# Kernel tuning notes

Measured on AMD Instinct MI355X. Metric: run time of the kernel, lower is better.

The kernel has to match this reference:

```python
import jax, jax.numpy as jnp
import numpy as np

D_I = 1024
D_O = 1024
B = 4
S = 4096

def setup_inputs() -> dict:
    key = jax.random.key(0)
    kx, kq, kk, kv = jax.random.split(key, 4)
    x = jax.random.normal(kx, (B, S, D_I), dtype=jnp.float32)
    # torch Linear(d_i, d_o) weight is [d_o, d_i]; we store transposed [d_i, d_o]
    sc = 1.0 / np.sqrt(D_I)
    Wq = jax.random.uniform(kq, (D_I, D_O), jnp.float32, -sc, sc)
    Wk = jax.random.uniform(kk, (D_I, D_O), jnp.float32, -sc, sc)
    Wv = jax.random.uniform(kv, (D_I, D_O), jnp.float32, -sc, sc)
    return {"x": x, "Wq": Wq, "Wk": Wk, "Wv": Wv}

def reference(x, Wq, Wk, Wv):
    # x: [B, S, d_i]
    q = jnp.einsum('bsd,de->bse', x, Wq)  # [B,S,d_o]
    k = jnp.einsum('bsd,de->bse', x, Wk)
    v = jnp.einsum('bsd,de->bse', x, Wv)
    scores = jnp.einsum('bqe,bke->bqk', q, k)  # [B,S,S]
    S_len = x.shape[1]
    causal = jnp.tril(jnp.ones((S_len, S_len), dtype=bool))  # keep lower tri
    scores = jnp.where(causal[None], scores, -jnp.inf)
    attn = jax.nn.softmax(scores / jnp.sqrt(jnp.float32(v.shape[-1])), axis=-1)
    # dropout p=0.0 -> identity
    return jnp.einsum('bqk,bke->bqe', attn, v)  # [B,S,d_o]
```

## Files before the change

### kernel.cpp

```cpp
#include <hip/hip_runtime.h>

typedef __bf16 bf16x8 __attribute__((ext_vector_type(8)));
typedef float f32x4 __attribute__((ext_vector_type(4)));

#define B_SZ 4
#define S_SZ 4096
#define D_SZ 1024
#define ELEMS_MAT ((size_t)B_SZ * S_SZ * D_SZ)

#define OFF_Q  ((size_t)0)
#define OFF_K  (ELEMS_MAT)
#define OFF_VT (2 * ELEMS_MAT)
#define ZONE   (3 * ELEMS_MAT)
#define OFF_XB (ZONE)
#define OFF_V  (ZONE + ELEMS_MAT)
#define OFF_WT (ZONE + 2 * ELEMS_MAT)
#define OFF_S  (ZONE)
#define S_BATCH ((size_t)8912896)

#define MFMA16(a, b, c) __builtin_amdgcn_mfma_f32_16x16x32_bf16((a), (b), (c), 0, 0, 0)

static __device__ __forceinline__ unsigned short f2bf(float f) {
  __bf16 h = (__bf16)f;
  return __builtin_bit_cast(unsigned short, h);
}

static __device__ __forceinline__ void async_lds16(const void* g, void* l) {
  __builtin_amdgcn_global_load_lds((__attribute__((address_space(1))) void*)g,
                                   (__attribute__((address_space(3))) void*)l, 16, 0, 0);
}

__global__ void cast_x_kernel(const float* __restrict__ x, unsigned short* __restrict__ xb) {
  size_t i = ((size_t)blockIdx.x * 256 + threadIdx.x) * 8;
  f32x4 a = *(const f32x4*)(x + i);
  f32x4 b = *(const f32x4*)(x + i + 4);
  bf16x8 o;
  o[0] = (__bf16)a[0]; o[1] = (__bf16)a[1]; o[2] = (__bf16)a[2]; o[3] = (__bf16)a[3];
  o[4] = (__bf16)b[0]; o[5] = (__bf16)b[1]; o[6] = (__bf16)b[2]; o[7] = (__bf16)b[3];
  *(bf16x8*)(xb + i) = o;
}

__global__ void cast_wt_kernel(const float* __restrict__ Wq, const float* __restrict__ Wk,
                               const float* __restrict__ Wv, unsigned short* __restrict__ Wt) {
  __shared__ float tl[64][65];
  const float* W = blockIdx.z == 0 ? Wq : (blockIdx.z == 1 ? Wk : Wv);
  unsigned short* out = Wt + (size_t)blockIdx.z * (size_t)D_SZ * (size_t)D_SZ;
  const int k0 = blockIdx.x * 64, n0 = blockIdx.y * 64;
  const int t = threadIdx.x;
  for (int i = t; i < 4096; i += 256) {
    int r = i >> 6, c = i & 63;
    tl[r][c] = W[(size_t)(k0 + r) * D_SZ + n0 + c];
  }
  __syncthreads();
  for (int i = t; i < 4096; i += 256) {
    int r = i >> 6, c = i & 63;
    out[(size_t)(n0 + r) * D_SZ + k0 + c] = f2bf(tl[c][r]);
  }
}

static __device__ __forceinline__ void stage_tile(const char* Asrc, size_t lda,
                                                  const char* Bsrc, size_t ldb,
                                                  unsigned short* ldsA, unsigned short* ldsB,
                                                  int tid) {
#pragma unroll
  for (int it = 0; it < 4; ++it) {
    int i = it * 512 + tid;
    int row = i >> 3;
    int scol = ((i & 7) ^ (row & 7)) << 4;
    async_lds16(Asrc + (size_t)row * lda + scol, (char*)ldsA + i * 16);
  }
#pragma unroll
  for (int it = 0; it < 4; ++it) {
    int i = it * 512 + tid;
    int row = i >> 3;
    int scol = ((i & 7) ^ (row & 7)) << 4;
    async_lds16(Bsrc + (size_t)row * ldb + scol, (char*)ldsB + i * 16);
  }
}

static __device__ __forceinline__ void compute_tile(const unsigned short* As,
                                                    const unsigned short* Bs,
                                                    int wm, int wn, int lr, int hi,
                                                    f32x4 acc[8][4]) {
  const char* Ab = (const char*)As;
  const char* Bb = (const char*)Bs;
#pragma unroll
  for (int q = 0; q < 4; ++q) {
    const int qm = q >> 1, qn = q & 1;
    bf16x8 af[4][2], bfr[2][2];
#pragma unroll
    for (int f = 0; f < 4; ++f) {
      const int r = wm * 128 + (qm * 4 + f) * 16 + lr;
#pragma unroll
      for (int kk = 0; kk < 2; ++kk)
        af[f][kk] = *(const bf16x8*)(Ab + r * 128 + ((kk * 64 + hi * 16) ^ ((r & 7) << 4)));
    }
#pragma unroll
    for (int f = 0; f < 2; ++f) {
      const int r = wn * 64 + (qn * 2 + f) * 16 + lr;
#pragma unroll
      for (int kk = 0; kk < 2; ++kk)
        bfr[f][kk] = *(const bf16x8*)(Bb + r * 128 + ((kk * 64 + hi * 16) ^ ((r & 7) << 4)));
    }
    __builtin_amdgcn_s_setprio(1);
#pragma unroll
    for (int kk = 0; kk < 2; ++kk)
#pragma unroll
      for (int f = 0; f < 4; ++f)
#pragma unroll
        for (int g = 0; g < 2; ++g)
          acc[qm * 4 + f][qn * 2 + g] = MFMA16(af[f][kk], bfr[g][kk], acc[qm * 4 + f][qn * 2 + g]);
    __builtin_amdgcn_s_setprio(0);
  }
}

static __device__ __forceinline__ void gemm_mainloop(const char* A, size_t lda,
                                                     const char* B, size_t ldb, int NT,
                                                     unsigned short sm[2][2][16384],
                                                     int tid, f32x4 acc[8][4]) {
  const int lane = tid & 63, w = tid >> 6;
  const int wm = w >> 2, wn = w & 3, lr = lane & 15, hi = lane >> 4;
  stage_tile(A, lda, B, ldb, sm[0][0], sm[0][1], tid);
  for (int t = 0; t < NT - 1; ++t) {
    const int cur = t & 1;
    stage_tile(A + (size_t)(t + 1) * 128, lda, B + (size_t)(t + 1) * 128, ldb,
               sm[cur ^ 1][0], sm[cur ^ 1][1], tid);
    asm volatile("s_waitcnt vmcnt(8)" ::: "memory");
    __builtin_amdgcn_s_barrier();
    compute_tile(sm[cur][0], sm[cur][1], wm, wn, lr, hi, acc);
    __builtin_amdgcn_s_barrier();
  }
  asm volatile("s_waitcnt vmcnt(0)" ::: "memory");
  __builtin_amdgcn_s_barrier();
  compute_tile(sm[(NT - 1) & 1][0], sm[(NT - 1) & 1][1], wm, wn, lr, hi, acc);
}

#define GEMM_PRE()                                    \
  __shared__ unsigned short sm[2][2][16384];          \
  const int tid = threadIdx.x;                        \
  f32x4 acc[8][4];                                    \
  {                                                   \
    const f32x4 z4 = {0.f, 0.f, 0.f, 0.f};            \
    _Pragma("unroll") for (int f = 0; f < 8; ++f)     \
      _Pragma("unroll") for (int g = 0; g < 4; ++g)   \
        acc[f][g] = z4;                               \
  }

#define EPI_IDX()                                     \
  const int lane = tid & 63, w = tid >> 6;            \
  const int wm = w >> 2, wn = w & 3;                  \
  const int lr = lane & 15, hi = lane >> 4;

__global__ __launch_bounds__(512, 2) void gemm_qkv256(const unsigned short* __restrict__ xb,
                                                      const unsigned short* __restrict__ Wt,
                                                      unsigned short* __restrict__ Q,
                                                      unsigned short* __restrict__ K,
                                                      unsigned short* __restrict__ V) {
  GEMM_PRE();
  const int bid = blockIdx.x;
  const int sw = (bid & 7) * 96 + (bid >> 3);
  const int mt = sw % 64, nt = sw / 64;
  const char* A = (const char*)xb + (size_t)mt * 256 * 2048;
  const char* Bp = (const char*)Wt + (size_t)nt * 256 * 2048;
  gemm_mainloop(A, 2048, Bp, 2048, 16, sm, tid, acc);
  EPI_IDX();
  unsigned short* Out = (nt >> 2) == 0 ? Q : ((nt >> 2) == 1 ? K : V);
  const int nb = (nt & 3) * 256;
#pragma unroll
  for (int f = 0; f < 8; ++f)
#pragma unroll
    for (int g = 0; g < 4; ++g)
#pragma unroll
      for (int j = 0; j < 4; ++j) {
        const int m = mt * 256 + wm * 128 + f * 16 + hi * 4 + j;
        const int n = nb + wn * 64 + g * 16 + lr;
        Out[(size_t)m * D_SZ + n] = f2bf(acc[f][g][j]);
      }
}

static __device__ __forceinline__ void stage_a256(const char* src, size_t ld, char* lds, int tid) {
#pragma unroll
  for (int it = 0; it < 4; ++it) {
    int i = it * 512 + tid;
    int row = i >> 3;
    int scol = ((i & 7) ^ (row & 7)) << 4;
    async_lds16(src + (size_t)row * ld + scol, lds + i * 16);
  }
}
static __device__ __forceinline__ void stage_b128(const char* src, size_t ld, char* lds, int tid) {
#pragma unroll
  for (int it = 0; it < 2; ++it) {
    int i = it * 512 + tid;
    int row = i >> 3;
    int scol = ((i & 7) ^ (row & 7)) << 4;
    async_lds16(src + (size_t)row * ld + scol, lds + i * 16);
  }
}

static __device__ __forceinline__ void compute_tile128(const unsigned short* As,
                                                       const unsigned short* Bs,
                                                       int wm, int wn, int lr, int hi,
                                                       f32x4 acc[8][2]) {
  const char* Ab = (const char*)As;
  const char* Bb = (const char*)Bs;
  bf16x8 bfr[2][2];
#pragma unroll
  for (int g = 0; g < 2; ++g) {
    const int r = wn * 32 + g * 16 + lr;
#pragma unroll
    for (int kk = 0; kk < 2; ++kk)
      bfr[g][kk] = *(const bf16x8*)(Bb + r * 128 + ((kk * 64 + hi * 16) ^ ((r & 7) << 4)));
  }
#pragma unroll
  for (int p = 0; p < 4; ++p) {
    bf16x8 af[2][2];
#pragma unroll
    for (int f = 0; f < 2; ++f) {
      const int r = wm * 128 + (p * 2 + f) * 16 + lr;
#pragma unroll
      for (int kk = 0; kk < 2; ++kk)
        af[f][kk] = *(const bf16x8*)(Ab + r * 128 + ((kk * 64 + hi * 16) ^ ((r & 7) << 4)));
    }
    __builtin_amdgcn_s_setprio(1);
#pragma unroll
    for (int kk = 0; kk < 2; ++kk)
#pragma unroll
      for (int f = 0; f < 2; ++f)
#pragma unroll
        for (int g = 0; g < 2; ++g)
          acc[p * 2 + f][g] = MFMA16(af[f][kk], bfr[g][kk], acc[p * 2 + f][g]);
    __builtin_amdgcn_s_setprio(0);
  }
}

static __device__ __forceinline__ void mainloop128(const char* A, size_t lda,
                                                   const char* B, size_t ldb, int NT,
                                                   unsigned short (*smA)[16384],
                                                   unsigned short (*smB)[8192],
                                                   int tid, f32x4 acc[8][2]) {
  const int lane = tid & 63, w = tid >> 6;
  const int wm = w >> 2, wn = w & 3, lr = lane & 15, hi = lane >> 4;
  stage_a256(A, lda, (char*)smA[0], tid);
  stage_b128(B, ldb, (char*)smB[0], tid);
  for (int t = 0; t < NT - 1; ++t) {
    const int cur = t & 1;
    stage_a256(A + (size_t)(t + 1) * 128, lda, (char*)smA[cur ^ 1], tid);
    stage_b128(B + (size_t)(t + 1) * 128, ldb, (char*)smB[cur ^ 1], tid);
    asm volatile("s_waitcnt vmcnt(6)" ::: "memory");
    __builtin_amdgcn_s_barrier();
    compute_tile128(smA[cur], smB[cur], wm, wn, lr, hi, acc);
    __builtin_amdgcn_s_barrier();
  }
  asm volatile("s_waitcnt vmcnt(0)" ::: "memory");
  __builtin_amdgcn_s_barrier();
  compute_tile128(smA[(NT - 1) & 1], smB[(NT - 1) & 1], wm, wn, lr, hi, acc);
}

__global__ void transpose_v_kernel(const unsigned short* __restrict__ V,
                                   unsigned short* __restrict__ Vt) {
  __shared__ unsigned short tl[64][65];
  const int s0 = blockIdx.x * 64, d0 = blockIdx.y * 64, b = blockIdx.z;
  const int t = threadIdx.x;
  const unsigned short* Vb = V + (size_t)b * S_SZ * D_SZ;
  unsigned short* Vo = Vt + (size_t)b * D_SZ * S_SZ;
  for (int i = t; i < 4096; i += 256) {
    int r = i >> 6, c = i & 63;
    tl[r][c] = Vb[(size_t)(s0 + r) * D_SZ + d0 + c];
  }
  __syncthreads();
  for (int i = t; i < 4096; i += 256) {
    int r = i >> 6, c = i & 63;
    Vo[(size_t)(d0 + r) * S_SZ + s0 + c] = tl[c][r];
  }
}

__global__ __launch_bounds__(512, 2) void s_gemm_bn128(const unsigned short* __restrict__ Q,
                                                       const unsigned short* __restrict__ K,
                                                       unsigned short* __restrict__ Sp) {
  __shared__ unsigned short smA[2][16384];
  __shared__ unsigned short smB[2][8192];
  const int tid = threadIdx.x;
  f32x4 acc[8][2];
  {
    const f32x4 z4 = {0.f, 0.f, 0.f, 0.f};
#pragma unroll
    for (int f = 0; f < 8; ++f)
#pragma unroll
      for (int g = 0; g < 2; ++g) acc[f][g] = z4;
  }
  const int bid = blockIdx.x;
  const int sw = (bid & 7) * 136 + (bid >> 3);
  const int b = sw / 272;
  const int r = sw % 272;
  int I = (int)((sqrtf(4.0f * r + 1.0f) - 1.0f) * 0.5f);
  while ((I + 1) * (I + 2) <= r) ++I;
  while (I * (I + 1) > r) --I;
  const int Jh = r - I * (I + 1);

  const char* A = (const char*)Q + ((size_t)b * S_SZ + (size_t)I * 256) * 2048;
  const char* Bp = (const char*)K + ((size_t)b * S_SZ + (size_t)Jh * 128) * 2048;
  mainloop128(A, 2048, Bp, 2048, 16, smA, smB, tid, acc);
  EPI_IDX();
  const int L = (I + 1) * 256;
  unsigned short* So = Sp + (size_t)b * S_BATCH + (size_t)(I * (I + 1) / 2) * 65536;
#pragma unroll
  for (int f = 0; f < 8; ++f)
#pragma unroll
    for (int g = 0; g < 2; ++g)
#pragma unroll
      for (int j = 0; j < 4; ++j) {
        const int m = wm * 128 + f * 16 + hi * 4 + j;
        const int n = Jh * 128 + wn * 32 + g * 16 + lr;
        float val = acc[f][g][j] * 0.03125f;
        if (n > I * 256 + m) val = -1e30f;
        So[(size_t)m * L + n] = f2bf(val);
      }
}

__global__ __launch_bounds__(256) void softmax_kernel(unsigned short* __restrict__ Sp) {
  const int w = threadIdx.x >> 6, lane = threadIdx.x & 63;
  const int rowflat = blockIdx.x * 4 + w;
  const int rr = 16383 - rowflat;
  const int b = rr >> 12, q = rr & 4095;
  const int I = q >> 8;
  const int L = (I + 1) << 8;
  unsigned short* base = Sp + (size_t)b * S_BATCH + (size_t)(I * (I + 1) / 2) * 65536 +
                         (size_t)(q & 255) * L;
  const int niter = (L + 511) >> 9;
  const __bf16 NEG = (__bf16)(-1e30f);
  bf16x8 v[8];
#pragma unroll
  for (int jt = 0; jt < 8; ++jt) {
    if (jt < niter) {
      const int off = jt * 512 + lane * 8;
      if (off < L) v[jt] = *(const bf16x8*)(base + off);
      else { bf16x8 fz; fz[0]=NEG;fz[1]=NEG;fz[2]=NEG;fz[3]=NEG;fz[4]=NEG;fz[5]=NEG;fz[6]=NEG;fz[7]=NEG; v[jt] = fz; }
    }
  }
  float m = -1e30f;
#pragma unroll
  for (int jt = 0; jt < 8; ++jt)
    if (jt < niter)
#pragma unroll
      for (int e = 0; e < 8; ++e) m = fmaxf(m, (float)v[jt][e]);
  m = fmaxf(m, __shfl_xor(m, 1));  m = fmaxf(m, __shfl_xor(m, 2));
  m = fmaxf(m, __shfl_xor(m, 4));  m = fmaxf(m, __shfl_xor(m, 8));
  m = fmaxf(m, __shfl_xor(m, 16)); m = fmaxf(m, __shfl_xor(m, 32));
  float l = 0.f;
#pragma unroll
  for (int jt = 0; jt < 8; ++jt)
    if (jt < niter)
#pragma unroll
      for (int e = 0; e < 8; ++e) l += __expf((float)v[jt][e] - m);
  l += __shfl_xor(l, 1);  l += __shfl_xor(l, 2);  l += __shfl_xor(l, 4);
  l += __shfl_xor(l, 8);  l += __shfl_xor(l, 16); l += __shfl_xor(l, 32);
  const float rl = 1.0f / l;
#pragma unroll
  for (int jt = 0; jt < 8; ++jt) {
    if (jt < niter) {
      const int off = jt * 512 + lane * 8;
      if (off < L) {
        bf16x8 p;
#pragma unroll
        for (int e = 0; e < 8; ++e) p[e] = (__bf16)(__expf((float)v[jt][e] - m) * rl);
        *(bf16x8*)(base + off) = p;
      }
    }
  }
}

__global__ __launch_bounds__(512, 2) void pv_bal(const unsigned short* __restrict__ Sp,
                                                 const unsigned short* __restrict__ Vt,
                                                 float* __restrict__ out) {
  __shared__ unsigned short smA[2][16384];
  __shared__ unsigned short smB[2][8192];
  const int tid = threadIdx.x;
  const int bid = blockIdx.x;
  const int sw = (bid & 7) * 32 + (bid >> 3);
  const int p = sw >> 5, b = (sw >> 3) & 3, nt = sw & 7;
  EPI_IDX();
  f32x4 acc[8][2];
#pragma unroll
  for (int half = 0; half < 2; ++half) {
    const int I = half ? (15 - p) : p;
    {
      const f32x4 z4 = {0.f, 0.f, 0.f, 0.f};
#pragma unroll
      for (int f = 0; f < 8; ++f)
#pragma unroll
        for (int g = 0; g < 2; ++g) acc[f][g] = z4;
    }
    const char* A = (const char*)(Sp + (size_t)b * S_BATCH + (size_t)(I * (I + 1) / 2) * 65536);
    const size_t lda = (size_t)(I + 1) * 512;
    const char* Bp = (const char*)Vt + ((size_t)b * D_SZ + (size_t)nt * 128) * (S_SZ * 2);
    mainloop128(A, lda, Bp, S_SZ * 2, (I + 1) * 4, smA, smB, tid, acc);
#pragma unroll
    for (int f = 0; f < 8; ++f)
#pragma unroll
      for (int g = 0; g < 2; ++g)
#pragma unroll
        for (int j = 0; j < 4; ++j) {
          const int m = wm * 128 + f * 16 + hi * 4 + j;
          const int n = nt * 128 + wn * 32 + g * 16 + lr;
          out[((size_t)b * S_SZ + (size_t)I * 256 + m) * D_SZ + n] = acc[f][g][j];
        }
    __syncthreads();
  }
}

extern "C" void kernel_launch(void* const* d_in, const int* in_sizes, int n_in,
                              void* d_out, int out_size, void* d_ws, size_t ws_size,
                              hipStream_t stream) {
  (void)in_sizes; (void)n_in; (void)out_size; (void)ws_size;
  const float* x  = (const float*)d_in[0];
  const float* Wq = (const float*)d_in[1];
  const float* Wk = (const float*)d_in[2];
  const float* Wv = (const float*)d_in[3];
  float* out = (float*)d_out;
  unsigned short* ws = (unsigned short*)d_ws;

  cast_x_kernel<<<8192, 256, 0, stream>>>(x, ws + OFF_XB);
  cast_wt_kernel<<<dim3(16, 16, 3), 256, 0, stream>>>(Wq, Wk, Wv, ws + OFF_WT);
  gemm_qkv256<<<768, 512, 0, stream>>>(ws + OFF_XB, ws + OFF_WT,
                                       ws + OFF_Q, ws + OFF_K, ws + OFF_V);
  transpose_v_kernel<<<dim3(64, 16, 4), 256, 0, stream>>>(ws + OFF_V, ws + OFF_VT);
  s_gemm_bn128<<<1088, 512, 0, stream>>>(ws + OFF_Q, ws + OFF_K, ws + OFF_S);
  softmax_kernel<<<4096, 256, 0, stream>>>(ws + OFF_S);
  pv_bal<<<256, 512, 0, stream>>>(ws + OFF_S, ws + OFF_VT, out);
}
```

Baseline: 406.3 us.

## Use 256x256 tiles for causal S GEMM and reshape warp tiling in GEMMs

```diff
diff --git a/kernel.cpp b/kernel.cpp
--- a/kernel.cpp
+++ b/kernel.cpp
@@ -84,10 +84,17 @@
                                                     f32x4 acc[8][4]) {
   const char* Ab = (const char*)As;
   const char* Bb = (const char*)Bs;
-#pragma unroll
-  for (int q = 0; q < 4; ++q) {
-    const int qm = q >> 1, qn = q & 1;
-    bf16x8 af[4][2], bfr[2][2];
+  bf16x8 bfr[4][2];
+#pragma unroll
+  for (int g = 0; g < 4; ++g) {
+    const int r = wn * 64 + g * 16 + lr;
+#pragma unroll
+    for (int kk = 0; kk < 2; ++kk)
+      bfr[g][kk] = *(const bf16x8*)(Bb + r * 128 + ((kk * 64 + hi * 16) ^ ((r & 7) << 4)));
+  }
+#pragma unroll
+  for (int qm = 0; qm < 2; ++qm) {
+    bf16x8 af[4][2];
 #pragma unroll
     for (int f = 0; f < 4; ++f) {
       const int r = wm * 128 + (qm * 4 + f) * 16 + lr;
@@ -95,21 +102,14 @@
       for (int kk = 0; kk < 2; ++kk)
         af[f][kk] = *(const bf16x8*)(Ab + r * 128 + ((kk * 64 + hi * 16) ^ ((r & 7) << 4)));
     }
-#pragma unroll
-    for (int f = 0; f < 2; ++f) {
-      const int r = wn * 64 + (qn * 2 + f) * 16 + lr;
-#pragma unroll
-      for (int kk = 0; kk < 2; ++kk)
-        bfr[f][kk] = *(const bf16x8*)(Bb + r * 128 + ((kk * 64 + hi * 16) ^ ((r & 7) << 4)));
-    }
     __builtin_amdgcn_s_setprio(1);
 #pragma unroll
     for (int kk = 0; kk < 2; ++kk)
 #pragma unroll
       for (int f = 0; f < 4; ++f)
 #pragma unroll
-        for (int g = 0; g < 2; ++g)
-          acc[qm * 4 + f][qn * 2 + g] = MFMA16(af[f][kk], bfr[g][kk], acc[qm * 4 + f][qn * 2 + g]);
+        for (int g = 0; g < 4; ++g)
+          acc[qm * 4 + f][g] = MFMA16(af[f][kk], bfr[g][kk], acc[qm * 4 + f][g]);
     __builtin_amdgcn_s_setprio(0);
   }
 }
@@ -178,84 +178,6 @@
       }
 }
 
-static __device__ __forceinline__ void stage_a256(const char* src, size_t ld, char* lds, int tid) {
-#pragma unroll
-  for (int it = 0; it < 4; ++it) {
-    int i = it * 512 + tid;
-    int row = i >> 3;
-    int scol = ((i & 7) ^ (row & 7)) << 4;
-    async_lds16(src + (size_t)row * ld + scol, lds + i * 16);
-  }
-}
-static __device__ __forceinline__ void stage_b128(const char* src, size_t ld, char* lds, int tid) {
-#pragma unroll
-  for (int it = 0; it < 2; ++it) {
-    int i = it * 512 + tid;
-    int row = i >> 3;
-    int scol = ((i & 7) ^ (row & 7)) << 4;
-    async_lds16(src + (size_t)row * ld + scol, lds + i * 16);
-  }
-}
-
-static __device__ __forceinline__ void compute_tile128(const unsigned short* As,
-                                                       const unsigned short* Bs,
-                                                       int wm, int wn, int lr, int hi,
-                                                       f32x4 acc[8][2]) {
-  const char* Ab = (const char*)As;
-  const char* Bb = (const char*)Bs;
-  bf16x8 bfr[2][2];
-#pragma unroll
-  for (int g = 0; g < 2; ++g) {
-    const int r = wn * 32 + g * 16 + lr;
-#pragma unroll
-    for (int kk = 0; kk < 2; ++kk)
-      bfr[g][kk] = *(const bf16x8*)(Bb + r * 128 + ((kk * 64 + hi * 16) ^ ((r & 7) << 4)));
-  }
-#pragma unroll
-  for (int p = 0; p < 4; ++p) {
-    bf16x8 af[2][2];
-#pragma unroll
-    for (int f = 0; f < 2; ++f) {
-      const int r = wm * 128 + (p * 2 + f) * 16 + lr;
-#pragma unroll
-      for (int kk = 0; kk < 2; ++kk)
-        af[f][kk] = *(const bf16x8*)(Ab + r * 128 + ((kk * 64 + hi * 16) ^ ((r & 7) << 4)));
-    }
-    __builtin_amdgcn_s_setprio(1);
-#pragma unroll
-    for (int kk = 0; kk < 2; ++kk)
-#pragma unroll
-      for (int f = 0; f < 2; ++f)
-#pragma unroll
-        for (int g = 0; g < 2; ++g)
-          acc[p * 2 + f][g] = MFMA16(af[f][kk], bfr[g][kk], acc[p * 2 + f][g]);
-    __builtin_amdgcn_s_setprio(0);
-  }
-}
-
-static __device__ __forceinline__ void mainloop128(const char* A, size_t lda,
-                                                   const char* B, size_t ldb, int NT,
-                                                   unsigned short (*smA)[16384],
-                                                   unsigned short (*smB)[8192],
-                                                   int tid, f32x4 acc[8][2]) {
-  const int lane = tid & 63, w = tid >> 6;
-  const int wm = w >> 2, wn = w & 3, lr = lane & 15, hi = lane >> 4;
-  stage_a256(A, lda, (char*)smA[0], tid);
-  stage_b128(B, ldb, (char*)smB[0], tid);
-  for (int t = 0; t < NT - 1; ++t) {
-    const int cur = t & 1;
-    stage_a256(A + (size_t)(t + 1) * 128, lda, (char*)smA[cur ^ 1], tid);
-    stage_b128(B + (size_t)(t + 1) * 128, ldb, (char*)smB[cur ^ 1], tid);
-    asm volatile("s_waitcnt vmcnt(6)" ::: "memory");
-    __builtin_amdgcn_s_barrier();
-    compute_tile128(smA[cur], smB[cur], wm, wn, lr, hi, acc);
-    __builtin_amdgcn_s_barrier();
-  }
-  asm volatile("s_waitcnt vmcnt(0)" ::: "memory");
-  __builtin_amdgcn_s_barrier();
-  compute_tile128(smA[(NT - 1) & 1], smB[(NT - 1) & 1], wm, wn, lr, hi, acc);
-}
-
 __global__ void transpose_v_kernel(const unsigned short* __restrict__ V,
                                    unsigned short* __restrict__ Vt) {
   __shared__ unsigned short tl[64][65];
@@ -274,43 +196,32 @@
   }
 }
 
-__global__ __launch_bounds__(512, 2) void s_gemm_bn128(const unsigned short* __restrict__ Q,
-                                                       const unsigned short* __restrict__ K,
-                                                       unsigned short* __restrict__ Sp) {
-  __shared__ unsigned short smA[2][16384];
-  __shared__ unsigned short smB[2][8192];
-  const int tid = threadIdx.x;
-  f32x4 acc[8][2];
-  {
-    const f32x4 z4 = {0.f, 0.f, 0.f, 0.f};
-#pragma unroll
-    for (int f = 0; f < 8; ++f)
-#pragma unroll
-      for (int g = 0; g < 2; ++g) acc[f][g] = z4;
-  }
+__global__ __launch_bounds__(512, 2) void s_gemm256(const unsigned short* __restrict__ Q,
+                                                    const unsigned short* __restrict__ K,
+                                                    unsigned short* __restrict__ Sp) {
+  GEMM_PRE();
   const int bid = blockIdx.x;
-  const int sw = (bid & 7) * 136 + (bid >> 3);
-  const int b = sw / 272;
-  const int r = sw % 272;
-  int I = (int)((sqrtf(4.0f * r + 1.0f) - 1.0f) * 0.5f);
-  while ((I + 1) * (I + 2) <= r) ++I;
-  while (I * (I + 1) > r) --I;
-  const int Jh = r - I * (I + 1);
-
+  const int sw = (bid & 7) * 68 + (bid >> 3);
+  const int b = sw / 136;
+  const int tile = sw % 136;
+  int I = (int)((sqrtf(8.0f * tile + 1.0f) - 1.0f) * 0.5f);
+  while ((I + 1) * (I + 2) / 2 <= tile) ++I;
+  while (I * (I + 1) / 2 > tile) --I;
+  const int J = tile - I * (I + 1) / 2;
   const char* A = (const char*)Q + ((size_t)b * S_SZ + (size_t)I * 256) * 2048;
-  const char* Bp = (const char*)K + ((size_t)b * S_SZ + (size_t)Jh * 128) * 2048;
-  mainloop128(A, 2048, Bp, 2048, 16, smA, smB, tid, acc);
+  const char* Bp = (const char*)K + ((size_t)b * S_SZ + (size_t)J * 256) * 2048;
+  gemm_mainloop(A, 2048, Bp, 2048, 16, sm, tid, acc);
   EPI_IDX();
   const int L = (I + 1) * 256;
   unsigned short* So = Sp + (size_t)b * S_BATCH + (size_t)(I * (I + 1) / 2) * 65536;
 #pragma unroll
   for (int f = 0; f < 8; ++f)
 #pragma unroll
-    for (int g = 0; g < 2; ++g)
+    for (int g = 0; g < 4; ++g)
 #pragma unroll
       for (int j = 0; j < 4; ++j) {
         const int m = wm * 128 + f * 16 + hi * 4 + j;
-        const int n = Jh * 128 + wn * 32 + g * 16 + lr;
+        const int n = J * 256 + wn * 64 + g * 16 + lr;
         float val = acc[f][g][j] * 0.03125f;
         if (n > I * 256 + m) val = -1e30f;
         So[(size_t)m * L + n] = f2bf(val);
@@ -369,6 +280,81 @@
   }
 }
 
+static __device__ __forceinline__ void stage_a256(const char* src, size_t ld, char* lds, int tid) {
+#pragma unroll
+  for (int it = 0; it < 4; ++it) {
+    int i = it * 512 + tid;
+    int row = i >> 3;
+    int scol = ((i & 7) ^ (row & 7)) << 4;
+    async_lds16(src + (size_t)row * ld + scol, lds + i * 16);
+  }
+}
+static __device__ __forceinline__ void stage_b128(const char* src, size_t ld, char* lds, int tid) {
+#pragma unroll
+  for (int it = 0; it < 2; ++it) {
+    int i = it * 512 + tid;
+    int row = i >> 3;
+    int scol = ((i & 7) ^ (row & 7)) << 4;
+    async_lds16(src + (size_t)row * ld + scol, lds + i * 16);
+  }
+}
+
+static __device__ __forceinline__ void compute_tile128(const unsigned short* As,
+                                                       const unsigned short* Bs,
+                                                       int wm, int wn, int lr, int hi,
+                                                       f32x4 acc[4][4]) {
+  const char* Ab = (const char*)As;
+  const char* Bb = (const char*)Bs;
+  bf16x8 bfr[4][2];
+#pragma unroll
+  for (int g = 0; g < 4; ++g) {
+    const int r = wn * 64 + g * 16 + lr;
+#pragma unroll
+    for (int kk = 0; kk < 2; ++kk)
+      bfr[g][kk] = *(const bf16x8*)(Bb + r * 128 + ((kk * 64 + hi * 16) ^ ((r & 7) << 4)));
+  }
+  bf16x8 af[4][2];
+#pragma unroll
+  for (int f = 0; f < 4; ++f) {
+    const int r = wm * 64 + f * 16 + lr;
+#pragma unroll
+    for (int kk = 0; kk < 2; ++kk)
+      af[f][kk] = *(const bf16x8*)(Ab + r * 128 + ((kk * 64 + hi * 16) ^ ((r & 7) << 4)));
+  }
+  __builtin_amdgcn_s_setprio(1);
+#pragma unroll
+  for (int kk = 0; kk < 2; ++kk)
+#pragma unroll
+    for (int f = 0; f < 4; ++f)
+#pragma unroll
+      for (int g = 0; g < 4; ++g)
+        acc[f][g] = MFMA16(af[f][kk], bfr[g][kk], acc[f][g]);
+  __builtin_amdgcn_s_setprio(0);
+}
+
+static __device__ __forceinline__ void mainloop128(const char* A, size_t lda,
+                                                   const char* B, size_t ldb, int NT,
+                                                   unsigned short (*smA)[16384],
+                                                   unsigned short (*smB)[8192],
+                                                   int tid, f32x4 acc[4][4]) {
+  const int lane = tid & 63, w = tid >> 6;
+  const int wm = w >> 1, wn = w & 1, lr = lane & 15, hi = lane >> 4;
+  stage_a256(A, lda, (char*)smA[0], tid);
+  stage_b128(B, ldb, (char*)smB[0], tid);
+  for (int t = 0; t < NT - 1; ++t) {
+    const int cur = t & 1;
+    stage_a256(A + (size_t)(t + 1) * 128, lda, (char*)smA[cur ^ 1], tid);
+    stage_b128(B + (size_t)(t + 1) * 128, ldb, (char*)smB[cur ^ 1], tid);
+    asm volatile("s_waitcnt vmcnt(6)" ::: "memory");
+    __builtin_amdgcn_s_barrier();
+    compute_tile128(smA[cur], smB[cur], wm, wn, lr, hi, acc);
+    __builtin_amdgcn_s_barrier();
+  }
+  asm volatile("s_waitcnt vmcnt(0)" ::: "memory");
+  __builtin_amdgcn_s_barrier();
+  compute_tile128(smA[(NT - 1) & 1], smB[(NT - 1) & 1], wm, wn, lr, hi, acc);
+}
+
 __global__ __launch_bounds__(512, 2) void pv_bal(const unsigned short* __restrict__ Sp,
                                                  const unsigned short* __restrict__ Vt,
                                                  float* __restrict__ out) {
@@ -378,30 +364,32 @@
   const int bid = blockIdx.x;
   const int sw = (bid & 7) * 32 + (bid >> 3);
   const int p = sw >> 5, b = (sw >> 3) & 3, nt = sw & 7;
-  EPI_IDX();
-  f32x4 acc[8][2];
+  const int lane = tid & 63, w = tid >> 6;
+  const int wm = w >> 1, wn = w & 1;
+  const int lr = lane & 15, hi = lane >> 4;
+  f32x4 acc[4][4];
 #pragma unroll
   for (int half = 0; half < 2; ++half) {
     const int I = half ? (15 - p) : p;
     {
       const f32x4 z4 = {0.f, 0.f, 0.f, 0.f};
 #pragma unroll
-      for (int f = 0; f < 8; ++f)
-#pragma unroll
-        for (int g = 0; g < 2; ++g) acc[f][g] = z4;
+      for (int f = 0; f < 4; ++f)
+#pragma unroll
+        for (int g = 0; g < 4; ++g) acc[f][g] = z4;
     }
     const char* A = (const char*)(Sp + (size_t)b * S_BATCH + (size_t)(I * (I + 1) / 2) * 65536);
     const size_t lda = (size_t)(I + 1) * 512;
     const char* Bp = (const char*)Vt + ((size_t)b * D_SZ + (size_t)nt * 128) * (S_SZ * 2);
     mainloop128(A, lda, Bp, S_SZ * 2, (I + 1) * 4, smA, smB, tid, acc);
 #pragma unroll
-    for (int f = 0; f < 8; ++f)
-#pragma unroll
-      for (int g = 0; g < 2; ++g)
+    for (int f = 0; f < 4; ++f)
+#pragma unroll
+      for (int g = 0; g < 4; ++g)
 #pragma unroll
         for (int j = 0; j < 4; ++j) {
-          const int m = wm * 128 + f * 16 + hi * 4 + j;
-          const int n = nt * 128 + wn * 32 + g * 16 + lr;
+          const int m = wm * 64 + f * 16 + hi * 4 + j;
+          const int n = nt * 128 + wn * 64 + g * 16 + lr;
           out[((size_t)b * S_SZ + (size_t)I * 256 + m) * D_SZ + n] = acc[f][g][j];
         }
     __syncthreads();
@@ -424,7 +412,7 @@
   gemm_qkv256<<<768, 512, 0, stream>>>(ws + OFF_XB, ws + OFF_WT,
                                        ws + OFF_Q, ws + OFF_K, ws + OFF_V);
   transpose_v_kernel<<<dim3(64, 16, 4), 256, 0, stream>>>(ws + OFF_V, ws + OFF_VT);
-  s_gemm_bn128<<<1088, 512, 0, stream>>>(ws + OFF_Q, ws + OFF_K, ws + OFF_S);
+  s_gemm256<<<544, 512, 0, stream>>>(ws + OFF_Q, ws + OFF_K, ws + OFF_S);
   softmax_kernel<<<4096, 256, 0, stream>>>(ws + OFF_S);
   pv_bal<<<256, 512, 0, stream>>>(ws + OFF_S, ws + OFF_VT, out);
 }
```

Measured after the change: 370.4 us. -8.8%, faster.
